# Kernel optimization log

Hardware: AMD Instinct MI355X
Metric: run time of the kernel (lower is better)

The kernel has to match this reference:

```python
import jax, jax.numpy as jnp
import numpy as np

SPIRAL_LEN = 12
V_LEVELS = [32768, 8192, 2048, 512, 128]
CHANNELS = [3, 32, 64, 128, 256]


def spiral_conv(x, spiral, W, b):
    # x: [B, V, C_in]; spiral: [V, S] neighbor indices
    B, V, C = x.shape
    g = x[:, spiral, :]                      # [B, V, S, C_in] irregular gather
    g = g.reshape(B, V, -1)                  # [B, V, S*C_in]
    return g @ W + b                         # [B, V, C_out]


def mesh_pool(x, idx, w):
    # sparse down_transform (<=3 nnz per row): out[b,i,:] = sum_k w[i,k] * x[b, idx[i,k], :]
    return jnp.einsum('bvkc,vk->bvc', x[:, idx, :], w)


def setup_inputs() -> dict:
    key = jax.random.key(0)
    ks = jax.random.split(key, 32)
    S = SPIRAL_LEN
    V = V_LEVELS
    C = CHANNELS
    d = {}
    d['x'] = jax.random.normal(ks[0], (32, V[0], C[0]), dtype=jnp.float32)
    for i in range(4):
        d[f'spiral{i}'] = jax.random.randint(ks[1 + i], (V[i], S), 0, V[i])
        d[f'didx{i}'] = jax.random.randint(ks[5 + i], (V[i + 1], 3), 0, V[i])
        w = jax.random.uniform(ks[9 + i], (V[i + 1], 3), dtype=jnp.float32)
        d[f'dw{i}'] = w / w.sum(-1, keepdims=True)  # barycentric-like rows
        fan_in = S * C[i]
        d[f'W{i}'] = jax.random.normal(ks[13 + i], (fan_in, C[i + 1]), dtype=jnp.float32) * np.float32(1.0 / np.sqrt(fan_in))
        d[f'b{i}'] = jnp.zeros((C[i + 1],), jnp.float32)
    flat_in = V[4] * C[4]  # num_vert * out_channels[-2]
    d['Wl1'] = jax.random.normal(ks[20], (flat_in, 512), dtype=jnp.float32) * np.float32(1.0 / np.sqrt(flat_in))
    d['bl1'] = jnp.zeros((512,), jnp.float32)
    d['Wl2'] = jax.random.normal(ks[21], (512, 64), dtype=jnp.float32) * np.float32(1.0 / np.sqrt(512))
    d['bl2'] = jnp.zeros((64,), jnp.float32)
    return d


def reference(x, spiral0, spiral1, spiral2, spiral3,
              didx0, didx1, didx2, didx3,
              dw0, dw1, dw2, dw3,
              W0, b0, W1, b1, W2, b2, W3, b3,
              Wl1, bl1, Wl2, bl2):
    spirals = (spiral0, spiral1, spiral2, spiral3)
    didx = (didx0, didx1, didx2, didx3)
    dw = (dw0, dw1, dw2, dw3)
    Wb = ((W0, b0), (W1, b1), (W2, b2), (W3, b3))
    for i in range(4):  # SpiralEnblock: elu(spiral_conv(x)) -> sparse pool
        x = jax.nn.elu(spiral_conv(x, spirals[i], *Wb[i]))
        x = mesh_pool(x, didx[i], dw[i])
    B = x.shape[0]
    x = x.reshape(B, -1)                     # [B, num_vert * C_last]
    x = jax.nn.elu(x @ Wl1 + bl1)            # [B, 512]
    y = x @ Wl2 + bl2                        # [B, latent]
    return (x, y)
```

## Files before the change

### kernel.cpp

```cpp
#include <hip/hip_runtime.h>
#include <cstdint>
#include <cstddef>

typedef _Float16 f16x8 __attribute__((ext_vector_type(8)));
typedef _Float16 f16x4 __attribute__((ext_vector_type(4)));
typedef float f32x4 __attribute__((ext_vector_type(4)));

static __device__ __forceinline__ float elu_f(float t) {
    return t > 0.0f ? t : expm1f(t);
}

typedef __attribute__((address_space(1))) const unsigned int guint;
typedef __attribute__((address_space(3))) unsigned int       luint;
static __device__ __forceinline__ void gload_lds16(const void* g, void* l)
{
    __builtin_amdgcn_global_load_lds((guint*)g, (luint*)l, 16, 0, 0);
}

static __device__ __forceinline__ int block_pu0(int bid, int P, int vshift_out, int nbl)
{
    if (nbl < 0) return bid * P;
    int xcd  = bid & 7;
    int slot = bid >> 3;
    int nb   = slot & ((1 << nbl) - 1);
    int tile = slot >> nbl;
    return ((xcd + (nb << 3)) << vshift_out) + tile * P;
}

template<int KTOT, int C_OUT, int BN>
__global__ __launch_bounds__(256)
void prep_w(const float* __restrict__ W, _Float16* __restrict__ o)
{
    constexpr int KT = KTOT/64;
    int i = blockIdx.x * 256 + threadIdx.x;
    if (i >= KTOT*C_OUT) return;
    int j = i & 7;
    int rest = i >> 3;
    int n = rest % BN;
    int kc = (rest / BN) & 7;
    int t = (rest / (BN*8)) % KT;
    int y = rest / (BN*8*KT);
    int k = t*64 + kc*8 + j;
    o[i] = (_Float16)W[(size_t)k*C_OUT + y*BN + n];
}

__global__ __launch_bounds__(256)
void prep_w0(const float* __restrict__ W, _Float16* __restrict__ o)
{
    int i = blockIdx.x * 256 + threadIdx.x;
    if (i >= 2048) return;
    int j = i & 7;
    int n = (i >> 3) & 31;
    int kc = i >> 8;
    int k = kc*8 + j;
    int s = k >> 2, c = k & 3;
    float v = (s < 12 && c < 3) ? W[(size_t)(s*3 + c)*32 + n] : 0.0f;
    o[i] = (_Float16)v;
}

__global__ __launch_bounds__(256)
void prep_xT(const float* __restrict__ x, _Float16* __restrict__ xT)
{
    __shared__ _Float16 t[16][64*4 + 8];
    const int v0 = blockIdx.x * 64;
    const int tid = threadIdx.x;
    #pragma unroll
    for (int it = 0; it < 4; ++it) {
        int e = it*256 + tid;
        int b = e >> 6, v = e & 63;
        const float* p = x + ((size_t)b*32768 + v0 + v)*3;
        f16x4 h;
        h[0] = (_Float16)p[0]; h[1] = (_Float16)p[1];
        h[2] = (_Float16)p[2]; h[3] = (_Float16)0.f;
        *(f16x4*)&t[b][v*4] = h;
    }
    __syncthreads();
    #pragma unroll
    for (int it = 0; it < 2; ++it) {
        int e = it*256 + tid;
        int vl = e >> 3, s = e & 7;
        f16x4 a = *(const f16x4*)&t[2*s][vl*4];
        f16x4 b = *(const f16x4*)&t[2*s+1][vl*4];
        f16x8 h;
        h[0]=a[0]; h[1]=a[1]; h[2]=a[2]; h[3]=a[3];
        h[4]=b[0]; h[5]=b[1]; h[6]=b[2]; h[7]=b[3];
        *(f16x8*)&xT[((size_t)(v0+vl)*16 + s*2)*4] = h;
    }
}

__global__ __launch_bounds__(256)
void prep_gidx(const int* __restrict__ didx, const int* __restrict__ spiral,
               unsigned int* __restrict__ g)
{
    int i = blockIdx.x*256 + threadIdx.x;
    if (i >= 24576*8) return;
    int q = i & 7;
    int row = i >> 3;
    unsigned int val = 0;
    if (q < 6) {
        int v = didx[row];
        unsigned int s0 = (unsigned int)spiral[v*12 + q*2];
        unsigned int s1 = (unsigned int)spiral[v*12 + q*2 + 1];
        val = s0 | (s1 << 16);
    }
    g[i] = val;
}

__global__ __launch_bounds__(256)
void conv0T(const _Float16* __restrict__ xT, const unsigned int* __restrict__ gidx,
            const _Float16* __restrict__ Wp, const float* __restrict__ bias,
            const float* __restrict__ dwt, _Float16* __restrict__ out)
{
    __shared__ _Float16 Ep[4][512];
    const int tid  = threadIdx.x;
    const int wave = tid >> 6;
    const int lane = tid & 63;
    const int quad = lane >> 4;
    const int l16  = lane & 15;
    const int u0   = blockIdx.x * 8 + wave * 2;

    f16x8 bf[2][2];
    #pragma unroll
    for (int kt = 0; kt < 2; ++kt)
        #pragma unroll
        for (int nt = 0; nt < 2; ++nt)
            bf[kt][nt] = *(const f16x8*)&Wp[(((kt*4+quad)*32) + nt*16 + l16)*8];
    float bv[2] = { bias[l16], bias[16 + l16] };

    #pragma unroll
    for (int ui = 0; ui < 2; ++ui) {
        int u = u0 + ui;
        f32x4 pacc[2] = {{0.f,0.f,0.f,0.f},{0.f,0.f,0.f,0.f}};
        #pragma unroll
        for (int kp = 0; kp < 3; ++kp) {
            int r = u*3 + kp;
            unsigned int gp0 = gidx[r*8 + quad];
            unsigned int gp1 = gidx[r*8 + 4 + quad];
            f16x4 a0 = *(const f16x4*)&xT[(size_t)(gp0 & 0xffffu)*64 + l16*4];
            f16x4 a1 = *(const f16x4*)&xT[(size_t)(gp0 >> 16)*64 + l16*4];
            f16x4 a2 = *(const f16x4*)&xT[(size_t)(gp1 & 0xffffu)*64 + l16*4];
            f16x4 a3 = *(const f16x4*)&xT[(size_t)(gp1 >> 16)*64 + l16*4];
            f16x8 af0, af1;
            af0[0]=a0[0]; af0[1]=a0[1]; af0[2]=a0[2]; af0[3]=a0[3];
            af0[4]=a1[0]; af0[5]=a1[1]; af0[6]=a1[2]; af0[7]=a1[3];
            af1[0]=a2[0]; af1[1]=a2[1]; af1[2]=a2[2]; af1[3]=a2[3];
            af1[4]=a3[0]; af1[5]=a3[1]; af1[6]=a3[2]; af1[7]=a3[3];
            float dw = dwt[r];
            #pragma unroll
            for (int nt = 0; nt < 2; ++nt) {
                f32x4 m = {0.f,0.f,0.f,0.f};
                m = __builtin_amdgcn_mfma_f32_16x16x32_f16(af0, bf[0][nt], m, 0,0,0);
                m = __builtin_amdgcn_mfma_f32_16x16x32_f16(af1, bf[1][nt], m, 0,0,0);
                #pragma unroll
                for (int rr = 0; rr < 4; ++rr)
                    pacc[nt][rr] += dw * elu_f(m[rr] + bv[nt]);
            }
        }
        #pragma unroll
        for (int nt = 0; nt < 2; ++nt)
            #pragma unroll
            for (int rr = 0; rr < 4; ++rr)
                Ep[wave][(quad*4+rr)*32 + nt*16 + l16] = (_Float16)pacc[nt][rr];
        int b  = lane >> 2;
        int c8 = lane & 3;
        f16x8 rowv = *(const f16x8*)&Ep[wave][b*32 + c8*8];
        *(f16x8*)&out[(size_t)b*262144 + (size_t)u*32 + c8*8] = rowv;
    }
}

template<int C_IN, int C_OUT, int P, int BN, int WGM, int WGN, bool OUT_HALF>
__global__ __launch_bounds__(256)
void conv_pool_mfma(const _Float16* __restrict__ x, const int* __restrict__ spiral,
                    const _Float16* __restrict__ Wp, const float* __restrict__ bias,
                    const int* __restrict__ didx, const float* __restrict__ dwt,
                    void* __restrict__ outv, int vshift_in, int vshift_out, int nbl)
{
    constexpr int R    = 3*P;
    constexpr int KTOT = 12*C_IN;
    constexpr int KT   = KTOT/64;
    constexpr int NST  = KT*2;
    constexpr int WTM  = R/WGM;
    constexpr int WTN  = BN/WGN;
    constexpr int NMT  = WTM/16;
    constexpr int NNT  = WTN/16;
    constexpr int C4   = BN/4;
    constexpr int GS   = (C_IN == 32) ? 1 : 2;
    constexpr int NG   = NST / GS;
    constexpr int CPR  = GS * 4;
    constexpr int CPRS = (CPR == 4) ? 2 : 3;
    constexpr int ACH  = R * CPR;
    constexpr int BCH  = GS * BN * 4;
    constexpr int AIPW = ACH / 256;
    constexpr int BIPW = BCH / 256;
    constexpr int ASUBH = R * GS * 32;
    constexpr int BSUBH = GS * 32 * BN;
    static_assert(WTM % 16 == 0 && WTN % 16 == 0, "tile");
    static_assert(R <= 256 && (P*C4) % 256 == 0, "loops");
    static_assert(ACH % 256 == 0 && BCH % 256 == 0, "stage");
    static_assert(NST % GS == 0 && GS*32 <= C_IN, "group");

    constexpr size_t BUFB = (size_t)(2*ASUBH + 2*BSUBH) * 2;
    constexpr size_t EB   = (size_t)R * (BN + 4) * 2;
    constexpr size_t GOFF = (BUFB > EB ? BUFB : EB);
    __shared__ __align__(16) char smem[GOFF + (size_t)R*12*2];
    _Float16* Ab = (_Float16*)smem;
    _Float16* Bb = (_Float16*)(smem + (size_t)2*ASUBH*2);
    unsigned short* gidx = (unsigned short*)(smem + GOFF);
    _Float16* E = (_Float16*)smem;

    const int tid  = threadIdx.x;
    const int wave = tid >> 6;
    const int lane = tid & 63;
    const int quad = lane >> 4;
    const int l16  = lane & 15;
    const int wm   = wave / WGN;
    const int wn   = wave % WGN;
    const int pu0  = block_pu0(blockIdx.x, P, vshift_out, nbl);
    const int n0   = blockIdx.y * BN;
    const int vmask_out = (1 << vshift_out) - 1;
    const int base_in = (pu0 >> vshift_out) << vshift_in;

    if (tid < R) {
        int ul = tid / 3;
        int kp = tid - ul*3;
        int u  = (pu0 + ul) & vmask_out;
        int v  = didx[u*3 + kp];
        const int* svp = spiral + v*12;
        #pragma unroll
        for (int j = 0; j < 12; ++j) gidx[tid*12 + j] = (unsigned short)svp[j];
    }
    __syncthreads();

    f32x4 acc[NMT][NNT];
    #pragma unroll
    for (int i = 0; i < NMT; ++i)
        #pragma unroll
        for (int j = 0; j < NNT; ++j) acc[i][j] = (f32x4){0.f, 0.f, 0.f, 0.f};

    const _Float16* xb = x + (size_t)base_in * C_IN;

    auto SWZ = [](int r) -> int {
        return (CPR == 4) ? ((r & 3) ^ ((r >> 2) & 3)) : (r & 7);
    };

    auto stage = [&](int g, int buf) {
        const int k0g = g * GS * 32;
        const int sv  = k0g / C_IN;
        const int c0  = k0g % C_IN;
        _Float16* Ad = Ab + (size_t)buf * ASUBH;
        #pragma unroll
        for (int i = 0; i < AIPW; ++i) {
            int t  = (wave*AIPW + i)*64 + lane;
            int r  = t >> CPRS;
            int q  = t & (CPR - 1);
            int qq = q ^ SWZ(r);
            int gr = gidx[r*12 + sv];
            gload_lds16(xb + (size_t)gr*C_IN + c0 + qq*8,
                        Ad + (size_t)(wave*AIPW + i)*512);
        }
        _Float16* Bd = Bb + (size_t)buf * BSUBH;
        const _Float16* bs = Wp + ((size_t)(blockIdx.y*NST + g*GS)*4)*BN*8;
        #pragma unroll
        for (int i = 0; i < BIPW; ++i) {
            int t = (wave*BIPW + i)*64 + lane;
            gload_lds16(bs + (size_t)t*8,
                        Bd + (size_t)(wave*BIPW + i)*512);
        }
    };

    stage(0, 0);
    __syncthreads();

    for (int g = 0; g < NG; ++g) {
        const int cur = g & 1;
        if (g + 1 < NG) stage(g + 1, cur ^ 1);
        const _Float16* Ar = Ab + (size_t)cur * ASUBH;
        const _Float16* Br = Bb + (size_t)cur * BSUBH;
        #pragma unroll
        for (int sl = 0; sl < GS; ++sl) {
            f16x8 af[NMT], bf[NNT];
            #pragma unroll
            for (int i = 0; i < NMT; ++i) {
                int m = wm*WTM + i*16 + l16;
                af[i] = *(const f16x8*)&Ar[(size_t)(m*CPR + ((sl*4 + quad) ^ SWZ(m)))*8];
            }
            #pragma unroll
            for (int j = 0; j < NNT; ++j) {
                int n = wn*WTN + j*16 + l16;
                bf[j] = *(const f16x8*)&Br[(size_t)((sl*4 + quad)*BN + n)*8];
            }
            #pragma unroll
            for (int i = 0; i < NMT; ++i)
                #pragma unroll
                for (int j = 0; j < NNT; ++j)
                    acc[i][j] = __builtin_amdgcn_mfma_f32_16x16x32_f16(
                        af[i], bf[j], acc[i][j], 0, 0, 0);
        }
        __syncthreads();
    }

    float bv[NNT];
    #pragma unroll
    for (int j = 0; j < NNT; ++j)
        bv[j] = bias[n0 + wn*WTN + j*16 + l16];

    #pragma unroll
    for (int i = 0; i < NMT; ++i) {
        int row_base = wm*WTM + i*16 + quad*4;
        #pragma unroll
        for (int j = 0; j < NNT; ++j) {
            int col = wn*WTN + j*16 + l16;
            #pragma unroll
            for (int r = 0; r < 4; ++r)
                E[(size_t)(row_base + r)*(BN+4) + col] =
                    (_Float16)elu_f(acc[i][j][r] + bv[j]);
        }
    }
    __syncthreads();

    #pragma unroll
    for (int e = tid; e < P*C4; e += 256) {
        int ul = e / C4;
        int c4 = e - ul*C4;
        int pu = pu0 + ul;
        int u  = pu & vmask_out;
        const float* w = dwt + u*3;
        f16x4 a0 = *(const f16x4*)&E[(size_t)(ul*3 + 0)*(BN+4) + c4*4];
        f16x4 a1 = *(const f16x4*)&E[(size_t)(ul*3 + 1)*(BN+4) + c4*4];
        f16x4 a2 = *(const f16x4*)&E[(size_t)(ul*3 + 2)*(BN+4) + c4*4];
        float ox = w[0]*(float)a0[0] + w[1]*(float)a1[0] + w[2]*(float)a2[0];
        float oy = w[0]*(float)a0[1] + w[1]*(float)a1[1] + w[2]*(float)a2[1];
        float oz = w[0]*(float)a0[2] + w[1]*(float)a1[2] + w[2]*(float)a2[2];
        float ow = w[0]*(float)a0[3] + w[1]*(float)a1[3] + w[2]*(float)a2[3];
        if (OUT_HALF) {
            f16x4 h; h[0]=(_Float16)ox; h[1]=(_Float16)oy; h[2]=(_Float16)oz; h[3]=(_Float16)ow;
            *(f16x4*)&((_Float16*)outv)[(size_t)pu*C_OUT + n0 + c4*4] = h;
        } else {
            float4 o; o.x=ox; o.y=oy; o.z=oz; o.w=ow;
            *(float4*)&((float*)outv)[(size_t)pu*C_OUT + n0 + c4*4] = o;
        }
    }
}

__global__ __launch_bounds__(256)
void fc1_partial(const float* __restrict__ xflat, const float* __restrict__ Wl1,
                 float* __restrict__ partial)
{
    __shared__ float sb[8704];
    const int tid = threadIdx.x;
    const int n4 = tid & 31;
    const int kq = (tid >> 5) & 3;
    const int mh = tid >> 7;
    const int nt = blockIdx.x;
    const int ks = blockIdx.y;
    const int kbase = ks * 128;

    for (int e = tid; e < 1024; e += 256) {
        int m = e >> 5, k4 = e & 31;
        *(float4*)&sb[m*128 + k4*4] = *(const float4*)&xflat[(size_t)m*32768 + kbase + k4*4];
    }
    __syncthreads();

    float acc[16][4];
    #pragma unroll
    for (int m = 0; m < 16; ++m)
        #pragma unroll
        for (int c = 0; c < 4; ++c) acc[m][c] = 0.0f;

    const float* Wb = Wl1 + (size_t)(kbase + kq*32)*512 + nt*128 + n4*4;
    #pragma unroll 2
    for (int i = 0; i < 32; i += 4) {
        float4 w0 = *(const float4*)(Wb + (size_t)(i+0)*512);
        float4 w1 = *(const float4*)(Wb + (size_t)(i+1)*512);
        float4 w2 = *(const float4*)(Wb + (size_t)(i+2)*512);
        float4 w3 = *(const float4*)(Wb + (size_t)(i+3)*512);
        #pragma unroll
        for (int m = 0; m < 16; ++m) {
            float4 xv = *(const float4*)&sb[(mh*16 + m)*128 + kq*32 + i];
            acc[m][0] += xv.x*w0.x + xv.y*w1.x + xv.z*w2.x + xv.w*w3.x;
            acc[m][1] += xv.x*w0.y + xv.y*w1.y + xv.z*w2.y + xv.w*w3.y;
            acc[m][2] += xv.x*w0.z + xv.y*w1.z + xv.z*w2.z + xv.w*w3.z;
            acc[m][3] += xv.x*w0.w + xv.y*w1.w + xv.z*w2.w + xv.w*w3.w;
        }
    }
    __syncthreads();

    int slot = (mh*2 + (kq >> 1))*32 + n4;
    if (kq & 1) {
        #pragma unroll
        for (int m = 0; m < 16; ++m)
            *(float4*)&sb[slot*68 + m*4] = *(float4*)&acc[m][0];
    }
    __syncthreads();
    if (!(kq & 1)) {
        #pragma unroll
        for (int m = 0; m < 16; ++m) {
            float4 v = *(const float4*)&sb[slot*68 + m*4];
            acc[m][0] += v.x; acc[m][1] += v.y; acc[m][2] += v.z; acc[m][3] += v.w;
        }
    }
    __syncthreads();
    int slot2 = mh*32 + n4;
    if (kq == 2) {
        #pragma unroll
        for (int m = 0; m < 16; ++m)
            *(float4*)&sb[slot2*68 + m*4] = *(float4*)&acc[m][0];
    }
    __syncthreads();
    if (kq == 0) {
        float* pb = partial + ((size_t)(ks*4 + nt)*32 + mh*16)*128 + n4*4;
        #pragma unroll
        for (int m = 0; m < 16; ++m) {
            float4 v = *(const float4*)&sb[slot2*68 + m*4];
            float4 o;
            o.x = acc[m][0] + v.x; o.y = acc[m][1] + v.y;
            o.z = acc[m][2] + v.z; o.w = acc[m][3] + v.w;
            *(float4*)(pb + (size_t)m*128) = o;
        }
    }
}

__global__ __launch_bounds__(256)
void fc1_reduce(const float* __restrict__ partial, const float* __restrict__ bl1,
                float* __restrict__ hout)
{
    int i = blockIdx.x * 256 + threadIdx.x;
    int m = i >> 9, n = i & 511;
    int nt = n >> 7, nl = n & 127;
    const float* p = partial + ((size_t)nt*32 + m)*128 + nl;
    float s = 0.0f;
    #pragma unroll 8
    for (int ks = 0; ks < 256; ++ks)
        s += p[(size_t)ks*4*4096];
    hout[i] = elu_f(s + bl1[n]);
}

__global__ __launch_bounds__(64)
void fc2_kernel(const float* __restrict__ h, const float* __restrict__ Wl2,
                const float* __restrict__ bl2, float* __restrict__ y)
{
    int m = blockIdx.x;
    int n = threadIdx.x;
    float s = bl2[n];
    for (int k = 0; k < 512; ++k)
        s += h[(size_t)m*512 + k] * Wl2[(size_t)k*64 + n];
    y[(size_t)m*64 + n] = s;
}

extern "C" void kernel_launch(void* const* d_in, const int* in_sizes, int n_in,
                              void* d_out, int out_size, void* d_ws, size_t ws_size,
                              hipStream_t stream)
{
    (void)in_sizes; (void)n_in; (void)out_size; (void)ws_size;

    const float* x0 = (const float*)d_in[0];
    const int*   sp[4]; const int* didx[4]; const float* dwp[4];
    const float* Wp[4]; const float* bp[4];
    for (int i = 0; i < 4; ++i) {
        sp[i]   = (const int*)  d_in[1 + i*5 + 0];
        didx[i] = (const int*)  d_in[1 + i*5 + 1];
        dwp[i]  = (const float*)d_in[1 + i*5 + 2];
        Wp[i]   = (const float*)d_in[1 + i*5 + 3];
        bp[i]   = (const float*)d_in[1 + i*5 + 4];
    }
    const float* Wl1 = (const float*)d_in[21];
    const float* bl1 = (const float*)d_in[22];
    const float* Wl2 = (const float*)d_in[23];
    const float* bl2 = (const float*)d_in[24];
    float* out = (float*)d_out;

    char* wsb = (char*)d_ws;
    float* persist      = (float*)wsb;
    float* partial      = (float*)(wsb + (4<<20));
    _Float16* xT        = (_Float16*)(wsb + (24<<20));
    _Float16* pooled0   = (_Float16*)(wsb + (32<<20));
    _Float16* pooled1   = (_Float16*)(wsb + (48<<20));
    _Float16* pooled2   = (_Float16*)(wsb + (56<<20));
    unsigned int* gidx0 = (unsigned int*)(wsb + (60<<20));
    _Float16* w0h       = (_Float16*)(wsb + (61<<20));
    _Float16* w1h       = w0h + 2048;
    _Float16* w2h       = w1h + 24576;
    _Float16* w3h       = w2h + 98304;

    prep_w0<<<8, 256, 0, stream>>>(Wp[0], w0h);
    prep_w< 384,  64,  64><<<( 24576 + 255)/256, 256, 0, stream>>>(Wp[1], w1h);
    prep_w< 768, 128, 128><<<( 98304 + 255)/256, 256, 0, stream>>>(Wp[2], w2h);
    prep_w<1536, 256,  64><<<(393216 + 255)/256, 256, 0, stream>>>(Wp[3], w3h);
    prep_gidx<<<768, 256, 0, stream>>>(didx[0], sp[0], gidx0);

    for (int h = 0; h < 2; ++h) {
        _Float16* xTh = xT + (size_t)h*2097152;
        prep_xT<<<512, 256, 0, stream>>>(x0 + (size_t)h*16*98304, xTh);
        conv0T<<<1024, 256, 0, stream>>>(xTh, gidx0, w0h, bp[0], dwp[0],
                                         pooled0 + (size_t)h*16*262144);
    }

    conv_pool_mfma<32,64,64,64,4,1,true><<<1024, 256, 0, stream>>>(
        pooled0, sp[1], w1h, bp[1], didx[1], dwp[1], pooled1, 13, 11, 2);

    conv_pool_mfma<64,128,32,128,2,2,true><<<512, 256, 0, stream>>>(
        pooled1, sp[2], w2h, bp[2], didx[2], dwp[2], pooled2, 11, 9, 2);

    conv_pool_mfma<128,256,32,64,2,2,false><<<dim3(128, 4), 256, 0, stream>>>(
        pooled2, sp[3], w3h, bp[3], didx[3], dwp[3], persist, 9, 7, 2);

    fc1_partial<<<dim3(4, 256), 256, 0, stream>>>(persist, Wl1, partial);
    fc1_reduce<<<64, 256, 0, stream>>>(partial, bl1, out);

    fc2_kernel<<<32, 64, 0, stream>>>(out, Wl2, bl2, out + 16384);
}
```

Measured before the change: 292.9 us.

## Triple-buffer LDS staging with explicit vmcnt waits and split layer-2 N tiles

Replaces the double-buffered global-to-LDS staging in the conv_pool MFMA kernel with a three-buffer pipeline that prefetches two stages ahead. It uses explicit s_waitcnt vmcnt and raw s_barrier calls instead of __syncthreads, so loads stay in flight across iterations and global load latency is hidden behind MFMA work. Layer 2 also changes from BN=128 to BN=64 with a 2-wide grid in y, which reduces LDS per block so three buffers fit and gives more blocks. The cost is more LDS per stage set and gathered A rows being reloaded for each N tile. Correctness depends on the hard-coded vmcnt literals matching the number of loads issued per stage.

```diff
diff --git a/kernel.cpp b/kernel.cpp
--- a/kernel.cpp
+++ b/kernel.cpp
@@ -15,6 +15,16 @@
 static __device__ __forceinline__ void gload_lds16(const void* g, void* l)
 {
     __builtin_amdgcn_global_load_lds((guint*)g, (luint*)l, 16, 0, 0);
+}
+
+template<int N>
+static __device__ __forceinline__ void vm_wait()
+{
+    static_assert(N == 0 || N == 4 || N == 5, "vmcnt literal");
+    if constexpr (N == 0)      asm volatile("s_waitcnt vmcnt(0)" ::: "memory");
+    else if constexpr (N == 4) asm volatile("s_waitcnt vmcnt(4)" ::: "memory");
+    else                       asm volatile("s_waitcnt vmcnt(5)" ::: "memory");
+    __builtin_amdgcn_sched_barrier(0);
 }
 
 static __device__ __forceinline__ int block_pu0(int bid, int P, int vshift_out, int nbl)
@@ -192,19 +202,23 @@
     constexpr int BCH  = GS * BN * 4;
     constexpr int AIPW = ACH / 256;
     constexpr int BIPW = BCH / 256;
+    constexpr int LPW  = AIPW + BIPW;
+    constexpr int NBUF = 3;
     constexpr int ASUBH = R * GS * 32;
     constexpr int BSUBH = GS * 32 * BN;
     static_assert(WTM % 16 == 0 && WTN % 16 == 0, "tile");
     static_assert(R <= 256 && (P*C4) % 256 == 0, "loops");
     static_assert(ACH % 256 == 0 && BCH % 256 == 0, "stage");
     static_assert(NST % GS == 0 && GS*32 <= C_IN, "group");
-
-    constexpr size_t BUFB = (size_t)(2*ASUBH + 2*BSUBH) * 2;
+    static_assert(NG >= 3, "pipeline depth");
+
+    constexpr size_t BUFB = (size_t)(NBUF*(ASUBH + BSUBH)) * 2;
     constexpr size_t EB   = (size_t)R * (BN + 4) * 2;
     constexpr size_t GOFF = (BUFB > EB ? BUFB : EB);
+    static_assert(GOFF + (size_t)R*12*2 <= 65536, "LDS budget");
     __shared__ __align__(16) char smem[GOFF + (size_t)R*12*2];
     _Float16* Ab = (_Float16*)smem;
-    _Float16* Bb = (_Float16*)(smem + (size_t)2*ASUBH*2);
+    _Float16* Bb = (_Float16*)(smem + (size_t)NBUF*ASUBH*2);
     unsigned short* gidx = (unsigned short*)(smem + GOFF);
     _Float16* E = (_Float16*)smem;
 
@@ -269,11 +283,17 @@
     };
 
     stage(0, 0);
-    __syncthreads();
+    stage(1, 1);
+    int cur = 0;
 
     for (int g = 0; g < NG; ++g) {
-        const int cur = g & 1;
-        if (g + 1 < NG) stage(g + 1, cur ^ 1);
+        if (g + 1 < NG) vm_wait<LPW>(); else vm_wait<0>();
+        __builtin_amdgcn_s_barrier();
+        __builtin_amdgcn_sched_barrier(0);
+
+        int nx2 = cur + 2; if (nx2 >= NBUF) nx2 -= NBUF;
+        if (g + 2 < NG) stage(g + 2, nx2);
+
         const _Float16* Ar = Ab + (size_t)cur * ASUBH;
         const _Float16* Br = Bb + (size_t)cur * BSUBH;
         #pragma unroll
@@ -296,7 +316,12 @@
                     acc[i][j] = __builtin_amdgcn_mfma_f32_16x16x32_f16(
                         af[i], bf[j], acc[i][j], 0, 0, 0);
         }
-        __syncthreads();
+
+        asm volatile("s_waitcnt lgkmcnt(0)" ::: "memory");
+        __builtin_amdgcn_sched_barrier(0);
+        __builtin_amdgcn_s_barrier();
+        __builtin_amdgcn_sched_barrier(0);
+        cur = (cur + 1 == NBUF) ? 0 : cur + 1;
     }
 
     float bv[NNT];
@@ -484,7 +509,7 @@
 
     prep_w0<<<8, 256, 0, stream>>>(Wp[0], w0h);
     prep_w< 384,  64,  64><<<( 24576 + 255)/256, 256, 0, stream>>>(Wp[1], w1h);
-    prep_w< 768, 128, 128><<<( 98304 + 255)/256, 256, 0, stream>>>(Wp[2], w2h);
+    prep_w< 768, 128,  64><<<( 98304 + 255)/256, 256, 0, stream>>>(Wp[2], w2h);
     prep_w<1536, 256,  64><<<(393216 + 255)/256, 256, 0, stream>>>(Wp[3], w3h);
     prep_gidx<<<768, 256, 0, stream>>>(didx[0], sp[0], gidx0);
 
@@ -498,7 +523,7 @@
     conv_pool_mfma<32,64,64,64,4,1,true><<<1024, 256, 0, stream>>>(
         pooled0, sp[1], w1h, bp[1], didx[1], dwp[1], pooled1, 13, 11, 2);
 
-    conv_pool_mfma<64,128,32,128,2,2,true><<<512, 256, 0, stream>>>(
+    conv_pool_mfma<64,128,32,64,2,2,true><<<dim3(512, 2), 256, 0, stream>>>(
         pooled1, sp[2], w2h, bp[2], didx[2], dwp[2], pooled2, 11, 9, 2);
 
     conv_pool_mfma<128,256,32,64,2,2,false><<<dim3(128, 4), 256, 0, stream>>>(
```

Result: slower. 302.0 us (+3.1%).
